# Kernel optimization log

Measured on AMD Instinct MI355X. Metric: run time of the kernel, lower is better.

## Reference

```python
import jax, jax.numpy as jnp
import numpy as np
import math

B, S, D, DH, R = 2, 2048, 1024, 64, 2


def _hex_grid(radius):
    coords = []
    for q in range(-radius, radius + 1):
        for r in range(max(-radius, -q - radius), min(radius, -q + radius) + 1):
            coords.append((q, r))
    return coords


def _adjacency(coords):
    idx = {c: i for i, c in enumerate(coords)}
    H = len(coords)
    A = np.zeros((H, H), dtype=np.float32)
    dirs = [(1, 0), (1, -1), (0, -1), (-1, 0), (-1, 1), (0, 1)]
    for (q, r), i in idx.items():
        for dq, dr in dirs:
            j = idx.get((q + dq, r + dr))
            if j is not None:
                A[i, j] = 1.0
    return A


def setup_inputs() -> dict:
    key = jax.random.key(0)
    ks = jax.random.split(key, 10)
    coords_list = _hex_grid(R)
    H = len(coords_list)  # 19 heads for radius 2
    coords = jnp.asarray(np.array(coords_list, dtype=np.float32))  # [H,2]
    A = _adjacency(coords_list) + np.eye(H, dtype=np.float32)      # self-loops
    adj_norm = jnp.asarray(A / A.sum(axis=1, keepdims=True))       # row-normalized [H,H]
    sd = 1.0 / math.sqrt(D)
    return {
        "x": jax.random.normal(ks[0], (B, S, D), jnp.float32),
        "coords": coords,
        "w_q": jax.random.normal(ks[1], (H, D, DH), jnp.float32) * sd,
        "w_k": jax.random.normal(ks[2], (H, D, DH), jnp.float32) * sd,
        "w_v": jax.random.normal(ks[3], (H, D, DH), jnp.float32) * sd,
        "wb1": jax.random.normal(ks[4], (2, D), jnp.float32) * 0.5,
        "bb1": jnp.zeros((D,), jnp.float32),
        "wb2": jax.random.normal(ks[5], (D, DH), jnp.float32) * sd,
        "bb2": jnp.zeros((DH,), jnp.float32),
        "w_mix": jax.random.normal(ks[6], (DH, DH), jnp.float32) / math.sqrt(DH),
        "adj_norm": adj_norm,
        "w_o": jax.random.normal(ks[7], (H * DH, D), jnp.float32) * sd,
    }


def reference(x, coords, w_q, w_k, w_v, wb1, bb1, wb2, bb2, w_mix, adj_norm, w_o):
    # coordinate bias: shared MLP mapping hex coord -> d_head bias, added to queries
    bias = jax.nn.relu(coords @ wb1 + bb1) @ wb2 + bb2          # [H,DH]
    # all heads vectorized: q/k/v [B,H,S,DH]
    q = jnp.einsum("bsd,hde->bhse", x, w_q) + bias[None, :, None, :]
    k = jnp.einsum("bsd,hde->bhse", x, w_k)
    v = jnp.einsum("bsd,hde->bhse", x, w_v)
    scores = jnp.einsum("bhse,bhte->bhst", q, k) / math.sqrt(DH)  # [B,H,S,S]
    attn = jax.nn.softmax(scores, axis=-1)
    heads = jnp.einsum("bhst,bhte->bhse", attn, v)               # [B,H,S,DH]
    # GNN mixing over the hex-grid adjacency (residual message passing)
    msg = jax.nn.relu(jnp.einsum("bhse,ef->bhsf", heads, w_mix))
    mixed = heads + jnp.einsum("hg,bgsf->bhsf", adj_norm, msg)   # [B,H,S,DH]
    # concat heads then output projection
    Bx, H, Sx, Dh = mixed.shape
    concat = jnp.transpose(mixed, (0, 2, 1, 3)).reshape(Bx, Sx, H * Dh)
    return concat @ w_o                                          # [B,S,D]
```

## Files before the change

### kernel.cpp

```cpp
#include <hip/hip_runtime.h>
#include <hip/hip_bf16.h>

#define H 19
#define Bv 2
#define Sv 2048
#define Dv 1024
#define DHv 64
#define KK2 (2*H*DHv)
#define QSCALE 0.125f

typedef __bf16 bf16x8 __attribute__((ext_vector_type(8)));
typedef float f32x4 __attribute__((ext_vector_type(4)));

__device__ __forceinline__ ushort f2bf(float f) {
    uint u = __float_as_uint(f);
    u = (u + 0x7fffu + ((u >> 16) & 1u)) >> 16;
    return (ushort)u;
}

__device__ __forceinline__ uint cvtpk(float lo, float hi) {
    uint r;
    asm("v_cvt_pk_bf16_f32 %0, %1, %2" : "=v"(r) : "v"(lo), "v"(hi));
    return r;
}

__device__ __forceinline__ void gll16(const ushort* g, ushort* l) {
    __builtin_amdgcn_global_load_lds(
        (const __attribute__((address_space(1))) unsigned int*)g,
        (__attribute__((address_space(3))) unsigned int*)l, 16, 0, 0);
}

__global__ __launch_bounds__(256) void prep_x(const float* __restrict__ x,
                                              ushort* __restrict__ xbf) {
    int idx = (blockIdx.x*256 + threadIdx.x)*8;
    float4 a = *(const float4*)&x[idx];
    float4 b = *(const float4*)&x[idx+4];
    uint4 o;
    o.x = cvtpk(a.x, a.y);
    o.y = cvtpk(a.z, a.w);
    o.z = cvtpk(b.x, b.y);
    o.w = cvtpk(b.z, b.w);
    *(uint4*)&xbf[idx] = o;
}

__global__ __launch_bounds__(256) void prep_w(const float* __restrict__ wq,
                                              const float* __restrict__ wk,
                                              const float* __restrict__ wv,
                                              ushort* __restrict__ wpackT) {
    const int dt = blockIdx.x, t = blockIdx.y, h = blockIdx.z;
    const float* w = (t == 0) ? wq : (t == 1) ? wk : wv;
    w += (size_t)h*Dv*DHv;
    __shared__ ushort T[64*65];
    const int tid = threadIdx.x;
    int row = tid >> 2, c4 = tid & 3;
    #pragma unroll
    for (int q4 = 0; q4 < 4; ++q4) {
        float4 v = *(const float4*)&w[(size_t)(dt*64+row)*DHv + c4*16 + q4*4];
        T[(c4*16 + q4*4 + 0)*65 + row] = f2bf(v.x);
        T[(c4*16 + q4*4 + 1)*65 + row] = f2bf(v.y);
        T[(c4*16 + q4*4 + 2)*65 + row] = f2bf(v.z);
        T[(c4*16 + q4*4 + 3)*65 + row] = f2bf(v.w);
    }
    __syncthreads();
    #pragma unroll
    for (int i = 0; i < 2; ++i) {
        int f = tid + i*256;
        int e = f >> 3, c = f & 7;
        uint u[4];
        #pragma unroll
        for (int j = 0; j < 4; ++j) {
            uint lo = T[e*65 + c*8 + 2*j];
            uint hi = T[e*65 + c*8 + 2*j + 1];
            u[j] = lo | (hi << 16);
        }
        *(uint4*)&wpackT[((size_t)h*192 + t*64 + e)*Dv + dt*64 + c*8] = make_uint4(u[0],u[1],u[2],u[3]);
    }
}

__global__ __launch_bounds__(256) void prep_wmix(const float* __restrict__ wm,
                                                 ushort* __restrict__ wmixT) {
    int tid = threadIdx.x;
    int e = tid >> 2, f4 = tid & 3;
    #pragma unroll
    for (int j = 0; j < 16; ++j) {
        int f = f4*16 + j;
        wmixT[e*64 + f] = f2bf(wm[f*64 + e]);
    }
}

__global__ __launch_bounds__(256) void prep_wo2(const float* __restrict__ wo,
                                                const float* __restrict__ adj,
                                                ushort* __restrict__ woTcat) {
    const int nt = blockIdx.x;
    const int g  = blockIdx.y;
    const int tid = threadIdx.x;
    const int e = tid >> 2, n4 = tid & 3;
    float acc[16];
    float part1[16];
    #pragma unroll
    for (int j = 0; j < 16; ++j) { acc[j] = 0.f; part1[j] = 0.f; }
    for (int h2 = 0; h2 < H; ++h2) {
        float a = adj[h2*H + g];
        const float* rp = wo + (size_t)(h2*64 + e)*Dv + nt*64 + n4*16;
        #pragma unroll
        for (int j4 = 0; j4 < 4; ++j4) {
            float4 v = *(const float4*)&rp[j4*4];
            acc[j4*4+0] += a*v.x; acc[j4*4+1] += a*v.y;
            acc[j4*4+2] += a*v.z; acc[j4*4+3] += a*v.w;
            if (h2 == g) {
                part1[j4*4+0] = v.x; part1[j4*4+1] = v.y;
                part1[j4*4+2] = v.z; part1[j4*4+3] = v.w;
            }
        }
    }
    #pragma unroll
    for (int j = 0; j < 16; ++j) {
        int n = nt*64 + n4*16 + j;
        woTcat[(size_t)n*KK2 + g*64 + e]            = f2bf(part1[j]);
        woTcat[(size_t)n*KK2 + H*DHv + g*64 + e]    = f2bf(acc[j]);
    }
}

__global__ void bias_kernel(const float* __restrict__ coords,
                            const float* __restrict__ wb1,
                            const float* __restrict__ bb1,
                            const float* __restrict__ wb2,
                            const float* __restrict__ bb2,
                            float* __restrict__ bias) {
    int h = blockIdx.x;
    int e = threadIdx.x;
    float c0 = coords[h*2 + 0];
    float c1 = coords[h*2 + 1];
    float acc = bb2[e];
    for (int d = 0; d < Dv; ++d) {
        float hd = c0*wb1[d] + c1*wb1[Dv + d] + bb1[d];
        hd = fmaxf(hd, 0.0f);
        acc += hd * wb2[d*DHv + e];
    }
    bias[h*DHv + e] = acc;
}

__global__ __launch_bounds__(256) void qkv_mfma(const ushort* __restrict__ xbf,
                                                const ushort* __restrict__ wpackT,
                                                const float* __restrict__ bias,
                                                ushort* __restrict__ qbf,
                                                ushort* __restrict__ kbf,
                                                ushort* __restrict__ vtbf) {
    const int mt = blockIdx.x, h = blockIdx.y;
    const int m0 = mt*64;
    const int tid = threadIdx.x;
    const int w = tid >> 6, lane = tid & 63;
    const int g = lane >> 4, r = lane & 15;

    __shared__ char lds[8192 + 24576];
    char* Xs = lds;
    char* Ws = lds + 8192;
    ushort* VtL = (ushort*)lds;

    f32x4 acc[4][3];
    const f32x4 zf = {0.f,0.f,0.f,0.f};
    #pragma unroll
    for (int m = 0; m < 4; ++m)
        #pragma unroll
        for (int n = 0; n < 3; ++n) acc[m][n] = zf;

    const ushort* xb = xbf + (size_t)m0*Dv;
    const ushort* wb = wpackT + (size_t)h*192*Dv;

    for (int kt = 0; kt < Dv; kt += 64) {
        __syncthreads();
        #pragma unroll
        for (int i = 0; i < 2; ++i) {
            int f = tid + i*256;
            int row = f >> 3, c = f & 7;
            *(bf16x8*)(Xs + row*128 + ((c*16) ^ ((row & 7) << 4))) =
                *(const bf16x8*)(xb + (size_t)row*Dv + kt + c*8);
        }
        #pragma unroll
        for (int i = 0; i < 6; ++i) {
            int f = tid + i*256;
            int row = f >> 3, c = f & 7;
            *(bf16x8*)(Ws + row*128 + ((c*16) ^ ((row & 7) << 4))) =
                *(const bf16x8*)(wb + (size_t)row*Dv + kt + c*8);
        }
        __syncthreads();
        #pragma unroll
        for (int kk = 0; kk < 2; ++kk) {
            bf16x8 a[4], bfr[3];
            #pragma unroll
            for (int m = 0; m < 4; ++m) {
                int row = m*16 + r;
                a[m] = *(const bf16x8*)(Xs + row*128 + (((kk*32 + g*8)*2) ^ ((row & 7) << 4)));
            }
            #pragma unroll
            for (int n = 0; n < 3; ++n) {
                int row = (w*3 + n)*16 + r;
                bfr[n] = *(const bf16x8*)(Ws + row*128 + (((kk*32 + g*8)*2) ^ ((row & 7) << 4)));
            }
            #pragma unroll
            for (int m = 0; m < 4; ++m)
                #pragma unroll
                for (int n = 0; n < 3; ++n)
                    acc[m][n] = __builtin_amdgcn_mfma_f32_16x16x32_bf16(a[m], bfr[n], acc[m][n], 0, 0, 0);
        }
    }

    __syncthreads();

    const int bb = m0 >> 11;
    const int s0 = m0 & 2047;
    #pragma unroll
    for (int m = 0; m < 4; ++m) {
        #pragma unroll
        for (int n = 0; n < 3; ++n) {
            int ng = w*3 + n;
            int t = ng >> 2;
            int e = (ng & 3)*16 + r;
            if (t == 0) {
                float bvv = bias[h*DHv + e];
                #pragma unroll
                for (int reg = 0; reg < 4; ++reg) {
                    int ss = s0 + m*16 + g*4 + reg;
                    qbf[(((size_t)bb*H + h)*Sv + ss)*DHv + e] = f2bf((acc[m][n][reg] + bvv)*QSCALE);
                }
            } else if (t == 1) {
                #pragma unroll
                for (int reg = 0; reg < 4; ++reg) {
                    int ss = s0 + m*16 + g*4 + reg;
                    kbf[(((size_t)bb*H + h)*Sv + ss)*DHv + e] = f2bf(acc[m][n][reg]);
                }
            } else {
                #pragma unroll
                for (int reg = 0; reg < 4; ++reg) {
                    int sl = m*16 + g*4 + reg;
                    VtL[e*66 + sl] = f2bf(acc[m][n][reg]);
                }
            }
        }
    }
    __syncthreads();
    #pragma unroll
    for (int i = 0; i < 2; ++i) {
        int f = tid + i*256;
        int dh = f >> 3, sc = f & 7;
        uint u[4];
        #pragma unroll
        for (int j = 0; j < 4; ++j) {
            uint lo = VtL[dh*66 + sc*8 + 2*j];
            uint hi = VtL[dh*66 + sc*8 + 2*j + 1];
            u[j] = lo | (hi << 16);
        }
        *(uint4*)&vtbf[(((size_t)bb*H + h)*DHv + dh)*Sv + s0 + sc*8] = make_uint4(u[0],u[1],u[2],u[3]);
    }
}

__global__ __launch_bounds__(256) void attn_mfma(const ushort* __restrict__ qg,
                                                 const ushort* __restrict__ kg,
                                                 const ushort* __restrict__ vtg,
                                                 ushort* __restrict__ headsbf) {
    const int qt = blockIdx.x, h = blockIdx.y, b = blockIdx.z;
    const int tid = threadIdx.x;
    const int w = tid >> 6, lane = tid & 63;
    const int g = lane >> 4, r = lane & 15;

    __shared__ ushort Ks[4096];
    __shared__ ushort Vs[4096];
    __shared__ ushort Ps[4][1024];

    const ushort* qb = qg + (((size_t)b*H + h)*Sv + qt*64 + w*16 + r)*DHv;
    const ushort* kb = kg + ((size_t)b*H + h)*Sv*DHv;
    const ushort* vb = vtg + ((size_t)b*H + h)*DHv*Sv;

    bf16x8 qf0 = *(const bf16x8*)(qb + g*8);
    bf16x8 qf1 = *(const bf16x8*)(qb + 32 + g*8);

    float m_run = -1e30f, l_run = 0.f;
    f32x4 o[4];
    const f32x4 zf = {0.f,0.f,0.f,0.f};
    o[0]=zf; o[1]=zf; o[2]=zf; o[3]=zf;

    const int srow = lane >> 3;
    const int scl  = lane & 7;

    for (int jt = 0; jt < Sv/64; ++jt) {
        __syncthreads();
        #pragma unroll
        for (int is = 0; is < 2; ++is) {
            int row = w*16 + is*8 + srow;
            int kcol = (scl ^ (row & 7)) * 8;
            gll16(kb + (size_t)(jt*64 + row)*DHv + kcol, &Ks[(w*16 + is*8)*64]);
            gll16(vb + (size_t)row*Sv + jt*64 + kcol, &Vs[(w*16 + is*8)*64]);
        }
        asm volatile("s_waitcnt vmcnt(0)" ::: "memory");
        __syncthreads();

        f32x4 sc[4];
        sc[0]=zf; sc[1]=zf; sc[2]=zf; sc[3]=zf;
        #pragma unroll
        for (int kk = 0; kk < 2; ++kk) {
            bf16x8 qf = kk ? qf1 : qf0;
            #pragma unroll
            for (int nt = 0; nt < 4; ++nt) {
                int kvrow = nt*16 + r;
                bf16x8 kf = *(const bf16x8*)((const char*)Ks + kvrow*128 +
                                             ((kk*64 + g*16) ^ ((kvrow & 7) << 4)));
                sc[nt] = __builtin_amdgcn_mfma_f32_16x16x32_bf16(kf, qf, sc[nt], 0, 0, 0);
            }
        }

        float pmax = sc[0][0];
        #pragma unroll
        for (int nt = 0; nt < 4; ++nt)
            #pragma unroll
            for (int reg = 0; reg < 4; ++reg)
                pmax = fmaxf(pmax, sc[nt][reg]);
        pmax = fmaxf(pmax, __shfl_xor(pmax, 16));
        pmax = fmaxf(pmax, __shfl_xor(pmax, 32));

        if (__any(pmax > m_run + 8.0f)) {
            float mn = fmaxf(m_run, pmax);
            float corr = __expf(m_run - mn);
            l_run *= corr;
            #pragma unroll
            for (int nt2 = 0; nt2 < 4; ++nt2) {
                o[nt2][0] *= corr; o[nt2][1] *= corr;
                o[nt2][2] *= corr; o[nt2][3] *= corr;
            }
            m_run = mn;
        }

        float lsum = 0.f;
        #pragma unroll
        for (int nt = 0; nt < 4; ++nt) {
            #pragma unroll
            for (int reg = 0; reg < 4; ++reg) {
                float p = __expf(sc[nt][reg] - m_run);
                sc[nt][reg] = p;
                lsum += p;
            }
        }
        lsum += __shfl_xor(lsum, 16);
        lsum += __shfl_xor(lsum, 32);
        l_run += lsum;

        ushort* pw = Ps[w];
        #pragma unroll
        for (int nt = 0; nt < 4; ++nt) {
            uint u0 = cvtpk(sc[nt][0], sc[nt][1]);
            uint u1 = cvtpk(sc[nt][2], sc[nt][3]);
            int chunk = (2*nt + (g >> 1)) ^ (r & 7);
            *(uint2*)((char*)pw + r*128 + (chunk << 4) + ((g & 1)*8)) = make_uint2(u0, u1);
        }

        #pragma unroll
        for (int kk = 0; kk < 2; ++kk) {
            bf16x8 pa = *(const bf16x8*)((const char*)pw + r*128 +
                                         (((kk*4 + g) ^ (r & 7)) << 4));
            #pragma unroll
            for (int nt2 = 0; nt2 < 4; ++nt2) {
                int dh = nt2*16 + r;
                bf16x8 vf = *(const bf16x8*)((const char*)Vs + dh*128 +
                                             ((kk*64 + g*16) ^ ((dh & 7) << 4)));
                o[nt2] = __builtin_amdgcn_mfma_f32_16x16x32_bf16(vf, pa, o[nt2], 0, 0, 0);
            }
        }
    }

    float inv = 1.0f / l_run;
    ushort* hp = headsbf + (((size_t)b*H + h)*Sv + qt*64 + w*16 + r)*DHv;
    #pragma unroll
    for (int nt2 = 0; nt2 < 4; ++nt2) {
        uint u0 = cvtpk(o[nt2][0]*inv, o[nt2][1]*inv);
        uint u1 = cvtpk(o[nt2][2]*inv, o[nt2][3]*inv);
        *(uint2*)(hp + nt2*16 + g*4) = make_uint2(u0, u1);
    }
}

__global__ __launch_bounds__(256) void msg_mfma(const ushort* __restrict__ headsbf,
                                                const ushort* __restrict__ wmixT,
                                                ushort* __restrict__ msgbf) {
    const int st = blockIdx.x, h = blockIdx.y, b = blockIdx.z;
    const int tid = threadIdx.x;
    const int w = tid >> 6, lane = tid & 63;
    const int g = lane >> 4, r = lane & 15;

    __shared__ ushort Hs[4096];
    __shared__ ushort Ws2[4096];

    const ushort* hb = headsbf + ((size_t)((size_t)b*H + h)*Sv + st*64)*DHv;
    const int srow = lane >> 3, scl = lane & 7;
    #pragma unroll
    for (int is = 0; is < 2; ++is) {
        int row = w*16 + is*8 + srow;
        int kcol = (scl ^ (row & 7)) * 8;
        gll16(hb + (size_t)row*DHv + kcol, &Hs[(w*16 + is*8)*64]);
        gll16(wmixT + (size_t)row*DHv + kcol, &Ws2[(w*16 + is*8)*64]);
    }
    asm volatile("s_waitcnt vmcnt(0)" ::: "memory");
    __syncthreads();

    f32x4 acc[4];
    const f32x4 zf = {0.f,0.f,0.f,0.f};
    acc[0]=zf; acc[1]=zf; acc[2]=zf; acc[3]=zf;
    #pragma unroll
    for (int kk = 0; kk < 2; ++kk) {
        int hrow = w*16 + r;
        bf16x8 hf = *(const bf16x8*)((const char*)Hs + hrow*128 +
                                     ((kk*64 + g*16) ^ ((hrow & 7) << 4)));
        #pragma unroll
        for (int nt = 0; nt < 4; ++nt) {
            int erow = nt*16 + r;
            bf16x8 wf = *(const bf16x8*)((const char*)Ws2 + erow*128 +
                                         ((kk*64 + g*16) ^ ((erow & 7) << 4)));
            acc[nt] = __builtin_amdgcn_mfma_f32_16x16x32_bf16(wf, hf, acc[nt], 0, 0, 0);
        }
    }
    ushort* mp = msgbf + ((size_t)((size_t)b*H + h)*Sv + st*64 + w*16 + r)*DHv;
    #pragma unroll
    for (int nt = 0; nt < 4; ++nt) {
        uint u0 = cvtpk(fmaxf(acc[nt][0], 0.f), fmaxf(acc[nt][1], 0.f));
        uint u1 = cvtpk(fmaxf(acc[nt][2], 0.f), fmaxf(acc[nt][3], 0.f));
        *(uint2*)(mp + nt*16 + g*4) = make_uint2(u0, u1);
    }
}

__global__ __launch_bounds__(256) void out_mfma(const ushort* __restrict__ headsbf,
                                                const ushort* __restrict__ msgbf,
                                                const ushort* __restrict__ woTcat,
                                                float* __restrict__ out) {
    const int mt = blockIdx.x, nt2 = blockIdx.y;
    const int m0 = mt*64, n0 = nt2*128;
    const int tid = threadIdx.x;
    const int w = tid >> 6, lane = tid & 63;
    const int g = lane >> 4, r = lane & 15;

    __shared__ char lds[8192 + 16384];
    char* As = lds;
    char* Bs = lds + 8192;

    const int b = m0 >> 11;
    const int s0 = m0 & 2047;

    f32x4 acc[8];
    const f32x4 zf = {0.f,0.f,0.f,0.f};
    #pragma unroll
    for (int n = 0; n < 8; ++n) acc[n] = zf;

    for (int ktile = 0; ktile < KK2/64; ++ktile) {
        const int hh = (ktile < H) ? ktile : ktile - H;
        const ushort* asrc = ((ktile < H) ? headsbf : msgbf) +
                             ((size_t)((size_t)b*H + hh)*Sv + s0)*DHv;
        __syncthreads();
        #pragma unroll
        for (int i = 0; i < 2; ++i) {
            int f = tid + i*256;
            int row = f >> 3, c = f & 7;
            *(bf16x8*)(As + row*128 + ((c*16) ^ ((row & 7) << 4))) =
                *(const bf16x8*)(asrc + (size_t)row*DHv + c*8);
        }
        #pragma unroll
        for (int i = 0; i < 4; ++i) {
            int f = tid + i*256;
            int row = f >> 3, c = f & 7;
            *(bf16x8*)(Bs + row*128 + ((c*16) ^ ((row & 7) << 4))) =
                *(const bf16x8*)(woTcat + (size_t)(n0 + row)*KK2 + ktile*64 + c*8);
        }
        __syncthreads();
        #pragma unroll
        for (int kk = 0; kk < 2; ++kk) {
            int arow = w*16 + r;
            bf16x8 a = *(const bf16x8*)(As + arow*128 + (((kk*32 + g*8)*2) ^ ((arow & 7) << 4)));
            #pragma unroll
            for (int n = 0; n < 8; ++n) {
                int brow = n*16 + r;
                bf16x8 bfr = *(const bf16x8*)(Bs + brow*128 + (((kk*32 + g*8)*2) ^ ((brow & 7) << 4)));
                acc[n] = __builtin_amdgcn_mfma_f32_16x16x32_bf16(a, bfr, acc[n], 0, 0, 0);
            }
        }
    }

    #pragma unroll
    for (int n = 0; n < 8; ++n) {
        #pragma unroll
        for (int reg = 0; reg < 4; ++reg) {
            int grow = m0 + w*16 + g*4 + reg;
            out[(size_t)grow*Dv + n0 + n*16 + r] = acc[n][reg];
        }
    }
}

extern "C" void kernel_launch(void* const* d_in, const int* in_sizes, int n_in,
                              void* d_out, int out_size, void* d_ws, size_t ws_size,
                              hipStream_t stream) {
    const float* x      = (const float*)d_in[0];
    const float* coords = (const float*)d_in[1];
    const float* w_q    = (const float*)d_in[2];
    const float* w_k    = (const float*)d_in[3];
    const float* w_v    = (const float*)d_in[4];
    const float* wb1    = (const float*)d_in[5];
    const float* bb1    = (const float*)d_in[6];
    const float* wb2    = (const float*)d_in[7];
    const float* bb2    = (const float*)d_in[8];
    const float* w_mix  = (const float*)d_in[9];
    const float* adj    = (const float*)d_in[10];
    const float* w_o    = (const float*)d_in[11];

    char* ws = (char*)d_ws;
    const size_t QKV_BYTES = (size_t)Bv*H*Sv*DHv*2;
    const size_t XBF_BYTES = (size_t)Bv*Sv*Dv*2;
    const size_t WPK_BYTES = (size_t)H*192*Dv*2;

    size_t off = 0;
    float*  bias  = (float*)(ws + off);  off += 16384;
    ushort* qbf   = (ushort*)(ws + off); off += QKV_BYTES;
    ushort* kbf   = (ushort*)(ws + off); off += QKV_BYTES;
    ushort* vtbf  = (ushort*)(ws + off); off += QKV_BYTES;
    ushort* hdbf  = (ushort*)(ws + off); off += QKV_BYTES;
    ushort* xbf   = (ushort*)(ws + off);
    ushort* msgbf = xbf;
    off += XBF_BYTES;
    ushort* wpkT  = (ushort*)(ws + off); off += WPK_BYTES;
    ushort* wmixT = (ushort*)(ws + off); off += 8192;
    ushort* woTc  = (ushort*)(ws + off); off += (size_t)Dv*KK2*2;
    float*  out   = (float*)d_out;

    prep_x<<<(Bv*Sv*Dv)/(256*8), 256, 0, stream>>>(x, xbf);
    prep_w<<<dim3(16, 3, H), 256, 0, stream>>>(w_q, w_k, w_v, wpkT);
    prep_wmix<<<1, 256, 0, stream>>>(w_mix, wmixT);
    prep_wo2<<<dim3(16, H), 256, 0, stream>>>(w_o, adj, woTc);
    bias_kernel<<<H, DHv, 0, stream>>>(coords, wb1, bb1, wb2, bb2, bias);
    qkv_mfma<<<dim3(64, H), 256, 0, stream>>>(xbf, wpkT, bias, qbf, kbf, vtbf);
    attn_mfma<<<dim3(Sv/64, H, Bv), 256, 0, stream>>>(qbf, kbf, vtbf, hdbf);
    msg_mfma<<<dim3(Sv/64, H, Bv), 256, 0, stream>>>(hdbf, wmixT, msgbf);
    out_mfma<<<dim3(64, 8), 256, 0, stream>>>(hdbf, msgbf, woTc, out);
}
```

Measured before the change: 346.8 us.

## Process 128 queries per attention block and fuse message MLP into epilogue

The attention kernel now handles two 16-row query groups per wave (128 queries per block), so each K/V tile loaded into LDS and each K/V fragment read into registers serves twice as many queries. The separate msg_mfma kernel is removed and its w_mix projection with ReLU is computed in the attention epilogue from the normalized heads held in LDS. This halves K/V global traffic per query and drops one launch plus the re-read of heads. In exchange it raises register pressure and halves the grid to 608 blocks, which may reduce occupancy.

```diff
diff --git a/kernel.cpp b/kernel.cpp
--- a/kernel.cpp
+++ b/kernel.cpp
@@ -257,7 +257,9 @@
 __global__ __launch_bounds__(256) void attn_mfma(const ushort* __restrict__ qg,
                                                  const ushort* __restrict__ kg,
                                                  const ushort* __restrict__ vtg,
-                                                 ushort* __restrict__ headsbf) {
+                                                 const ushort* __restrict__ wmixT,
+                                                 ushort* __restrict__ headsbf,
+                                                 ushort* __restrict__ msgbf) {
     const int qt = blockIdx.x, h = blockIdx.y, b = blockIdx.z;
     const int tid = threadIdx.x;
     const int w = tid >> 6, lane = tid & 63;
@@ -265,19 +267,27 @@
 
     __shared__ ushort Ks[4096];
     __shared__ ushort Vs[4096];
-    __shared__ ushort Ps[4][1024];
-
-    const ushort* qb = qg + (((size_t)b*H + h)*Sv + qt*64 + w*16 + r)*DHv;
-    const ushort* kb = kg + ((size_t)b*H + h)*Sv*DHv;
-    const ushort* vb = vtg + ((size_t)b*H + h)*DHv*Sv;
-
-    bf16x8 qf0 = *(const bf16x8*)(qb + g*8);
-    bf16x8 qf1 = *(const bf16x8*)(qb + 32 + g*8);
-
-    float m_run = -1e30f, l_run = 0.f;
-    f32x4 o[4];
+    __shared__ ushort Ps[4][2048];
+
+    const size_t bh = (size_t)b*H + h;
+    const ushort* kb = kg + bh*Sv*DHv;
+    const ushort* vb = vtg + bh*DHv*Sv;
+
+    bf16x8 qf[2][2];
+    #pragma unroll
+    for (int grp = 0; grp < 2; ++grp) {
+        const ushort* qb = qg + (bh*Sv + qt*128 + w*32 + grp*16 + r)*DHv;
+        qf[grp][0] = *(const bf16x8*)(qb + g*8);
+        qf[grp][1] = *(const bf16x8*)(qb + 32 + g*8);
+    }
+
+    float m_run[2] = {-1e30f, -1e30f}, l_run[2] = {0.f, 0.f};
+    f32x4 o[2][4];
     const f32x4 zf = {0.f,0.f,0.f,0.f};
-    o[0]=zf; o[1]=zf; o[2]=zf; o[3]=zf;
+    #pragma unroll
+    for (int grp = 0; grp < 2; ++grp)
+        #pragma unroll
+        for (int n = 0; n < 4; ++n) o[grp][n] = zf;
 
     const int srow = lane >> 3;
     const int scl  = lane & 7;
@@ -294,133 +304,142 @@
         asm volatile("s_waitcnt vmcnt(0)" ::: "memory");
         __syncthreads();
 
-        f32x4 sc[4];
-        sc[0]=zf; sc[1]=zf; sc[2]=zf; sc[3]=zf;
-        #pragma unroll
-        for (int kk = 0; kk < 2; ++kk) {
-            bf16x8 qf = kk ? qf1 : qf0;
+        bf16x8 kf[2][4];
+        #pragma unroll
+        for (int kk = 0; kk < 2; ++kk)
             #pragma unroll
             for (int nt = 0; nt < 4; ++nt) {
                 int kvrow = nt*16 + r;
-                bf16x8 kf = *(const bf16x8*)((const char*)Ks + kvrow*128 +
-                                             ((kk*64 + g*16) ^ ((kvrow & 7) << 4)));
-                sc[nt] = __builtin_amdgcn_mfma_f32_16x16x32_bf16(kf, qf, sc[nt], 0, 0, 0);
-            }
-        }
-
-        float pmax = sc[0][0];
+                kf[kk][nt] = *(const bf16x8*)((const char*)Ks + kvrow*128 +
+                                              ((kk*64 + g*16) ^ ((kvrow & 7) << 4)));
+            }
+
+        f32x4 sc[2][4];
+        #pragma unroll
+        for (int grp = 0; grp < 2; ++grp) {
+            sc[grp][0]=zf; sc[grp][1]=zf; sc[grp][2]=zf; sc[grp][3]=zf;
+            #pragma unroll
+            for (int kk = 0; kk < 2; ++kk)
+                #pragma unroll
+                for (int nt = 0; nt < 4; ++nt)
+                    sc[grp][nt] = __builtin_amdgcn_mfma_f32_16x16x32_bf16(
+                        kf[kk][nt], qf[grp][kk], sc[grp][nt], 0, 0, 0);
+        }
+
+        #pragma unroll
+        for (int grp = 0; grp < 2; ++grp) {
+            float pmax = sc[grp][0][0];
+            #pragma unroll
+            for (int nt = 0; nt < 4; ++nt)
+                #pragma unroll
+                for (int reg = 0; reg < 4; ++reg)
+                    pmax = fmaxf(pmax, sc[grp][nt][reg]);
+            pmax = fmaxf(pmax, __shfl_xor(pmax, 16));
+            pmax = fmaxf(pmax, __shfl_xor(pmax, 32));
+
+            if (__any(pmax > m_run[grp] + 8.0f)) {
+                float mn = fmaxf(m_run[grp], pmax);
+                float corr = __expf(m_run[grp] - mn);
+                l_run[grp] *= corr;
+                #pragma unroll
+                for (int nt2 = 0; nt2 < 4; ++nt2) {
+                    o[grp][nt2][0] *= corr; o[grp][nt2][1] *= corr;
+                    o[grp][nt2][2] *= corr; o[grp][nt2][3] *= corr;
+                }
+                m_run[grp] = mn;
+            }
+
+            float lsum = 0.f;
+            #pragma unroll
+            for (int nt = 0; nt < 4; ++nt) {
+                #pragma unroll
+                for (int reg = 0; reg < 4; ++reg) {
+                    float p = __expf(sc[grp][nt][reg] - m_run[grp]);
+                    sc[grp][nt][reg] = p;
+                    lsum += p;
+                }
+            }
+            lsum += __shfl_xor(lsum, 16);
+            lsum += __shfl_xor(lsum, 32);
+            l_run[grp] += lsum;
+
+            ushort* pw = &Ps[w][grp*1024];
+            #pragma unroll
+            for (int nt = 0; nt < 4; ++nt) {
+                uint u0 = cvtpk(sc[grp][nt][0], sc[grp][nt][1]);
+                uint u1 = cvtpk(sc[grp][nt][2], sc[grp][nt][3]);
+                int chunk = (2*nt + (g >> 1)) ^ (r & 7);
+                *(uint2*)((char*)pw + r*128 + (chunk << 4) + ((g & 1)*8)) = make_uint2(u0, u1);
+            }
+        }
+
+        bf16x8 vf[2][4];
+        #pragma unroll
+        for (int kk = 0; kk < 2; ++kk)
+            #pragma unroll
+            for (int nt2 = 0; nt2 < 4; ++nt2) {
+                int dh = nt2*16 + r;
+                vf[kk][nt2] = *(const bf16x8*)((const char*)Vs + dh*128 +
+                                               ((kk*64 + g*16) ^ ((dh & 7) << 4)));
+            }
+
+        #pragma unroll
+        for (int grp = 0; grp < 2; ++grp) {
+            const ushort* pw = &Ps[w][grp*1024];
+            #pragma unroll
+            for (int kk = 0; kk < 2; ++kk) {
+                bf16x8 pa = *(const bf16x8*)((const char*)pw + r*128 +
+                                             (((kk*4 + g) ^ (r & 7)) << 4));
+                #pragma unroll
+                for (int nt2 = 0; nt2 < 4; ++nt2)
+                    o[grp][nt2] = __builtin_amdgcn_mfma_f32_16x16x32_bf16(
+                        vf[kk][nt2], pa, o[grp][nt2], 0, 0, 0);
+            }
+        }
+    }
+
+    #pragma unroll
+    for (int grp = 0; grp < 2; ++grp) {
+        float inv = 1.0f / l_run[grp];
+        ushort* hp = headsbf + (bh*Sv + qt*128 + w*32 + grp*16 + r)*DHv;
+        ushort* pw = &Ps[w][grp*1024];
+        #pragma unroll
+        for (int nt2 = 0; nt2 < 4; ++nt2) {
+            uint u0 = cvtpk(o[grp][nt2][0]*inv, o[grp][nt2][1]*inv);
+            uint u1 = cvtpk(o[grp][nt2][2]*inv, o[grp][nt2][3]*inv);
+            *(uint2*)(hp + nt2*16 + g*4) = make_uint2(u0, u1);
+            int chunk = (2*nt2 + (g >> 1)) ^ (r & 7);
+            *(uint2*)((char*)pw + r*128 + (chunk << 4) + ((g & 1)*8)) = make_uint2(u0, u1);
+        }
+    }
+
+    bf16x8 wm[2][4];
+    #pragma unroll
+    for (int kk = 0; kk < 2; ++kk)
         #pragma unroll
         for (int nt = 0; nt < 4; ++nt)
-            #pragma unroll
-            for (int reg = 0; reg < 4; ++reg)
-                pmax = fmaxf(pmax, sc[nt][reg]);
-        pmax = fmaxf(pmax, __shfl_xor(pmax, 16));
-        pmax = fmaxf(pmax, __shfl_xor(pmax, 32));
-
-        if (__any(pmax > m_run + 8.0f)) {
-            float mn = fmaxf(m_run, pmax);
-            float corr = __expf(m_run - mn);
-            l_run *= corr;
-            #pragma unroll
-            for (int nt2 = 0; nt2 < 4; ++nt2) {
-                o[nt2][0] *= corr; o[nt2][1] *= corr;
-                o[nt2][2] *= corr; o[nt2][3] *= corr;
-            }
-            m_run = mn;
-        }
-
-        float lsum = 0.f;
-        #pragma unroll
-        for (int nt = 0; nt < 4; ++nt) {
-            #pragma unroll
-            for (int reg = 0; reg < 4; ++reg) {
-                float p = __expf(sc[nt][reg] - m_run);
-                sc[nt][reg] = p;
-                lsum += p;
-            }
-        }
-        lsum += __shfl_xor(lsum, 16);
-        lsum += __shfl_xor(lsum, 32);
-        l_run += lsum;
-
-        ushort* pw = Ps[w];
-        #pragma unroll
-        for (int nt = 0; nt < 4; ++nt) {
-            uint u0 = cvtpk(sc[nt][0], sc[nt][1]);
-            uint u1 = cvtpk(sc[nt][2], sc[nt][3]);
-            int chunk = (2*nt + (g >> 1)) ^ (r & 7);
-            *(uint2*)((char*)pw + r*128 + (chunk << 4) + ((g & 1)*8)) = make_uint2(u0, u1);
-        }
-
+            wm[kk][nt] = *(const bf16x8*)(wmixT + (nt*16 + r)*64 + kk*32 + g*8);
+
+    #pragma unroll
+    for (int grp = 0; grp < 2; ++grp) {
+        const ushort* pw = &Ps[w][grp*1024];
+        f32x4 macc[4];
+        macc[0]=zf; macc[1]=zf; macc[2]=zf; macc[3]=zf;
         #pragma unroll
         for (int kk = 0; kk < 2; ++kk) {
             bf16x8 pa = *(const bf16x8*)((const char*)pw + r*128 +
                                          (((kk*4 + g) ^ (r & 7)) << 4));
             #pragma unroll
-            for (int nt2 = 0; nt2 < 4; ++nt2) {
-                int dh = nt2*16 + r;
-                bf16x8 vf = *(const bf16x8*)((const char*)Vs + dh*128 +
-                                             ((kk*64 + g*16) ^ ((dh & 7) << 4)));
-                o[nt2] = __builtin_amdgcn_mfma_f32_16x16x32_bf16(vf, pa, o[nt2], 0, 0, 0);
-            }
-        }
-    }
-
-    float inv = 1.0f / l_run;
-    ushort* hp = headsbf + (((size_t)b*H + h)*Sv + qt*64 + w*16 + r)*DHv;
-    #pragma unroll
-    for (int nt2 = 0; nt2 < 4; ++nt2) {
-        uint u0 = cvtpk(o[nt2][0]*inv, o[nt2][1]*inv);
-        uint u1 = cvtpk(o[nt2][2]*inv, o[nt2][3]*inv);
-        *(uint2*)(hp + nt2*16 + g*4) = make_uint2(u0, u1);
-    }
-}
-
-__global__ __launch_bounds__(256) void msg_mfma(const ushort* __restrict__ headsbf,
-                                                const ushort* __restrict__ wmixT,
-                                                ushort* __restrict__ msgbf) {
-    const int st = blockIdx.x, h = blockIdx.y, b = blockIdx.z;
-    const int tid = threadIdx.x;
-    const int w = tid >> 6, lane = tid & 63;
-    const int g = lane >> 4, r = lane & 15;
-
-    __shared__ ushort Hs[4096];
-    __shared__ ushort Ws2[4096];
-
-    const ushort* hb = headsbf + ((size_t)((size_t)b*H + h)*Sv + st*64)*DHv;
-    const int srow = lane >> 3, scl = lane & 7;
-    #pragma unroll
-    for (int is = 0; is < 2; ++is) {
-        int row = w*16 + is*8 + srow;
-        int kcol = (scl ^ (row & 7)) * 8;
-        gll16(hb + (size_t)row*DHv + kcol, &Hs[(w*16 + is*8)*64]);
-        gll16(wmixT + (size_t)row*DHv + kcol, &Ws2[(w*16 + is*8)*64]);
-    }
-    asm volatile("s_waitcnt vmcnt(0)" ::: "memory");
-    __syncthreads();
-
-    f32x4 acc[4];
-    const f32x4 zf = {0.f,0.f,0.f,0.f};
-    acc[0]=zf; acc[1]=zf; acc[2]=zf; acc[3]=zf;
-    #pragma unroll
-    for (int kk = 0; kk < 2; ++kk) {
-        int hrow = w*16 + r;
-        bf16x8 hf = *(const bf16x8*)((const char*)Hs + hrow*128 +
-                                     ((kk*64 + g*16) ^ ((hrow & 7) << 4)));
+            for (int nt = 0; nt < 4; ++nt)
+                macc[nt] = __builtin_amdgcn_mfma_f32_16x16x32_bf16(wm[kk][nt], pa, macc[nt], 0, 0, 0);
+        }
+        ushort* mp = msgbf + (bh*Sv + qt*128 + w*32 + grp*16 + r)*DHv;
         #pragma unroll
         for (int nt = 0; nt < 4; ++nt) {
-            int erow = nt*16 + r;
-            bf16x8 wf = *(const bf16x8*)((const char*)Ws2 + erow*128 +
-                                         ((kk*64 + g*16) ^ ((erow & 7) << 4)));
-            acc[nt] = __builtin_amdgcn_mfma_f32_16x16x32_bf16(wf, hf, acc[nt], 0, 0, 0);
-        }
-    }
-    ushort* mp = msgbf + ((size_t)((size_t)b*H + h)*Sv + st*64 + w*16 + r)*DHv;
-    #pragma unroll
-    for (int nt = 0; nt < 4; ++nt) {
-        uint u0 = cvtpk(fmaxf(acc[nt][0], 0.f), fmaxf(acc[nt][1], 0.f));
-        uint u1 = cvtpk(fmaxf(acc[nt][2], 0.f), fmaxf(acc[nt][3], 0.f));
-        *(uint2*)(mp + nt*16 + g*4) = make_uint2(u0, u1);
+            uint u0 = cvtpk(fmaxf(macc[nt][0], 0.f), fmaxf(macc[nt][1], 0.f));
+            uint u1 = cvtpk(fmaxf(macc[nt][2], 0.f), fmaxf(macc[nt][3], 0.f));
+            *(uint2*)(mp + nt*16 + g*4) = make_uint2(u0, u1);
+        }
     }
 }
 
@@ -530,7 +549,6 @@
     prep_wo2<<<dim3(16, H), 256, 0, stream>>>(w_o, adj, woTc);
     bias_kernel<<<H, DHv, 0, stream>>>(coords, wb1, bb1, wb2, bb2, bias);
     qkv_mfma<<<dim3(64, H), 256, 0, stream>>>(xbf, wpkT, bias, qbf, kbf, vtbf);
-    attn_mfma<<<dim3(Sv/64, H, Bv), 256, 0, stream>>>(qbf, kbf, vtbf, hdbf);
-    msg_mfma<<<dim3(Sv/64, H, Bv), 256, 0, stream>>>(hdbf, wmixT, msgbf);
+    attn_mfma<<<dim3(Sv/128, H, Bv), 256, 0, stream>>>(qbf, kbf, vtbf, wmixT, hdbf, msgbf);
     out_mfma<<<dim3(64, 8), 256, 0, stream>>>(hdbf, msgbf, woTc, out);
 }
```

After: 371.5 us. 7.1% more time.
